# Kernel tuning notes

Hardware: AMD Instinct MI355X
Metric: run time of the kernel (lower is better)

The kernel has to match this reference:

```python
import jax, jax.numpy as jnp
import numpy as np

DIM = 1024
HEADS = 16
HEAD_DIM = DIM // HEADS
SCALE = HEAD_DIM ** -0.5
B, N = 2, 2048


def setup_inputs() -> dict:
    key = jax.random.key(0)
    ks = jax.random.split(key, 12)
    s = DIM ** -0.5
    return {
        "x_real": jax.random.normal(ks[0], (B, N, DIM), jnp.float32),
        "x_imag": jax.random.normal(ks[1], (B, N, DIM), jnp.float32),
        "Wqkv_r": jax.random.normal(ks[2], (3 * DIM, DIM), jnp.float32) * s,
        "bqkv_r": jax.random.normal(ks[3], (3 * DIM,), jnp.float32) * 0.01,
        "Wqkv_i": jax.random.normal(ks[4], (3 * DIM, DIM), jnp.float32) * s,
        "bqkv_i": jax.random.normal(ks[5], (3 * DIM,), jnp.float32) * 0.01,
        "Wout_r": jax.random.normal(ks[6], (DIM, DIM), jnp.float32) * s,
        "bout_r": jax.random.normal(ks[7], (DIM,), jnp.float32) * 0.01,
        "Wout_i": jax.random.normal(ks[8], (DIM, DIM), jnp.float32) * s,
        "bout_i": jax.random.normal(ks[9], (DIM,), jnp.float32) * 0.01,
    }


def _split_heads(qkv):
    # (B, N, 3*D) -> q, k, v each (B, H, N, hd)
    b, n, _ = qkv.shape
    qkv = qkv.reshape(b, n, 3, HEADS, HEAD_DIM).transpose(2, 0, 3, 1, 4)
    return qkv[0], qkv[1], qkv[2]


def reference(x_real, x_imag, Wqkv_r, bqkv_r, Wqkv_i, bqkv_i,
              Wout_r, bout_r, Wout_i, bout_i):
    b, n, d = x_real.shape
    q_r, k_r, v_r = _split_heads(x_real @ Wqkv_r.T + bqkv_r)
    q_i, k_i, v_i = _split_heads(x_imag @ Wqkv_i.T + bqkv_i)

    # complex score: (q_r + i q_i) (k_r - i k_i)^T pattern per source
    attn_real = (jnp.einsum('bhqd,bhkd->bhqk', q_r, k_r)
                 + jnp.einsum('bhqd,bhkd->bhqk', q_i, k_i)) * SCALE
    attn_imag = (jnp.einsum('bhqd,bhkd->bhqk', q_i, k_r)
                 - jnp.einsum('bhqd,bhkd->bhqk', q_r, k_i)) * SCALE
    attn_mag = jnp.sqrt(attn_real ** 2 + attn_imag ** 2)
    w = jax.nn.softmax(attn_mag, axis=-1)

    out_r = jnp.einsum('bhqk,bhkd->bhqd', w, v_r).transpose(0, 2, 1, 3).reshape(b, n, d)
    out_i = jnp.einsum('bhqk,bhkd->bhqd', w, v_i).transpose(0, 2, 1, 3).reshape(b, n, d)
    out_r = out_r @ Wout_r.T + bout_r
    out_i = out_i @ Wout_i.T + bout_i
    return out_r, out_i
```

## Files before the change

kernel.cpp:

```cpp
#include <hip/hip_runtime.h>


#define DIM_   1024
#define HEADS_ 16
#define HD_    64
#define BB_    2
#define NN_    2048
#define MTOT_  (BB_*NN_)
#define SCALE_ 0.125f

typedef __bf16 bf16;
typedef __bf16 bf16x8 __attribute__((ext_vector_type(8)));
typedef short  s16x8  __attribute__((ext_vector_type(8)));
typedef float  fx4    __attribute__((ext_vector_type(4)));

__device__ __forceinline__ bf16x8 neg8(bf16x8 v) {
    s16x8 s;
    __builtin_memcpy(&s, &v, sizeof(s));
    s ^= (short)0x8000;
    bf16x8 r;
    __builtin_memcpy(&r, &s, sizeof(r));
    return r;
}

__device__ __forceinline__ void gl_lds16(const void* g, void* l) {
    __builtin_amdgcn_global_load_lds(
        (const __attribute__((address_space(1))) unsigned int*)g,
        (__attribute__((address_space(3))) unsigned int*)l, 16, 0, 0);
}

__global__ __launch_bounds__(256) void qkv_gemm(
    const float* __restrict__ xr, const float* __restrict__ xi,
    const float* __restrict__ Wr, const float* __restrict__ Wi,
    const float* __restrict__ br, const float* __restrict__ bi,
    bf16* __restrict__ qbuf, bf16* __restrict__ kbuf, bf16* __restrict__ vbuf)
{
    const int z = blockIdx.z;
    const float* __restrict__ A    = z ? xi : xr;
    const float* __restrict__ W    = z ? Wi : Wr;
    const float* __restrict__ bias = z ? bi : br;
    const int n0 = blockIdx.x * 128;
    const int m0 = blockIdx.y * 128;

    __shared__ bf16 As[128*40];
    __shared__ bf16 Bs[128*40];

    const int tid  = threadIdx.x;
    const int w    = tid >> 6, lane = tid & 63;
    const int quad = lane >> 4, lc = lane & 15;
    const int wm   = (w >> 1) * 64, wn = (w & 1) * 64;

    const fx4 fzero = {0.f, 0.f, 0.f, 0.f};
    fx4 acc[4][4];
#pragma unroll
    for (int mi = 0; mi < 4; ++mi)
#pragma unroll
        for (int ni = 0; ni < 4; ++ni) acc[mi][ni] = fzero;

    for (int k0 = 0; k0 < DIM_; k0 += 32) {
#pragma unroll
        for (int it = 0; it < 2; ++it) {
            int flat = it*2048 + tid*8;
            int row = flat >> 5, col = flat & 31;
            const float* pa = A + (size_t)(m0+row)*DIM_ + k0 + col;
            const float* pb = W + (size_t)(n0+row)*DIM_ + k0 + col;
            fx4 a0 = *(const fx4*)pa, a1 = *(const fx4*)(pa+4);
            fx4 b0 = *(const fx4*)pb, b1 = *(const fx4*)(pb+4);
            bf16x8 av, bv;
#pragma unroll
            for (int j = 0; j < 4; ++j) {
                av[j] = (bf16)a0[j]; av[j+4] = (bf16)a1[j];
                bv[j] = (bf16)b0[j]; bv[j+4] = (bf16)b1[j];
            }
            *(bf16x8*)&As[row*40 + col] = av;
            *(bf16x8*)&Bs[row*40 + col] = bv;
        }
        __syncthreads();

        bf16x8 af[4], bfr[4];
#pragma unroll
        for (int mi = 0; mi < 4; ++mi) af[mi]  = *(bf16x8*)&As[(wm + mi*16 + lc)*40 + quad*8];
#pragma unroll
        for (int ni = 0; ni < 4; ++ni) bfr[ni] = *(bf16x8*)&Bs[(wn + ni*16 + lc)*40 + quad*8];
#pragma unroll
        for (int mi = 0; mi < 4; ++mi)
#pragma unroll
            for (int ni = 0; ni < 4; ++ni)
                acc[mi][ni] = __builtin_amdgcn_mfma_f32_16x16x32_bf16(af[mi], bfr[ni], acc[mi][ni], 0, 0, 0);
        __syncthreads();
    }

#pragma unroll
    for (int mi = 0; mi < 4; ++mi)
#pragma unroll
        for (int ni = 0; ni < 4; ++ni)
#pragma unroll
            for (int r = 0; r < 4; ++r) {
                int gm = m0 + wm + mi*16 + quad*4 + r;
                int gc = n0 + wn + ni*16 + lc;
                float val = acc[mi][ni][r] + bias[gc];
                bf16 bv = (bf16)val;
                int which = gc >> 10, h = (gc >> 6) & 15, hd = gc & 63;
                int b = gm >> 11, n = gm & 2047;
                size_t base = (size_t)((z*BB_ + b)*HEADS_ + h);
                if (which == 0)      qbuf[(base*NN_ + n)*HD_ + hd] = bv;
                else if (which == 1) kbuf[(base*NN_ + n)*HD_ + hd] = bv;
                else                 vbuf[(base*HD_ + hd)*NN_ + n] = bv;
            }
}

#define KT 32
#define NSTEP (NN_/KT)

__global__ __launch_bounds__(256, 2) void attn_fwd(
    const bf16* __restrict__ qbuf, const bf16* __restrict__ kbuf,
    const bf16* __restrict__ vbuf, bf16* __restrict__ obuf)
{
    const int bid = blockIdx.x;
    const int xcd = bid & 7;
    const int i   = bid >> 3;
    const int hb  = xcd*4 + (i >> 4);
    const int blk = i & 15;
    const int b = hb >> 4, h = hb & 15;

    const int tid  = threadIdx.x;
    const int w    = tid >> 6, lane = tid & 63;
    const int quad = lane >> 4, lc = lane & 15;
    const int q0   = blk*128 + w*32;

    __shared__ __align__(16) bf16 KV[2*8192];
    __shared__ __align__(16) bf16 Ps[4*2*32*40];
    bf16* psw = Ps + w*(2*32*40);

    const size_t hR = (size_t)(b)*HEADS_ + h;
    const size_t hI = (size_t)(BB_ + b)*HEADS_ + h;
    const bf16* qrg = qbuf + hR*NN_*HD_;
    const bf16* qig = qbuf + hI*NN_*HD_;
    const char* krg = (const char*)(kbuf + hR*NN_*HD_);
    const char* kig = (const char*)(kbuf + hI*NN_*HD_);
    const char* vrg = (const char*)(vbuf + hR*HD_*NN_);
    const char* vig = (const char*)(vbuf + hI*HD_*NN_);

    bf16x8 qr0[2], qr1[2], qi0[2], qi1[2], nqr0[2], nqr1[2];
#pragma unroll
    for (int band = 0; band < 2; ++band) {
        const bf16* pr = qrg + (size_t)(q0 + band*16 + lc)*HD_ + quad*8;
        const bf16* pi = qig + (size_t)(q0 + band*16 + lc)*HD_ + quad*8;
        qr0[band] = *(const bf16x8*)(pr);
        qr1[band] = *(const bf16x8*)(pr + 32);
        qi0[band] = *(const bf16x8*)(pi);
        qi1[band] = *(const bf16x8*)(pi + 32);
        nqr0[band] = neg8(qr0[band]);
        nqr1[band] = neg8(qr1[band]);
    }

    const char* stg_base;
    size_t lane_off, step_mul, j_mul;
    if (w < 2) {
        stg_base = w ? kig : krg;
        lane_off = (size_t)(lane >> 3)*128 + (size_t)((lane & 7) ^ (lane >> 3))*16;
        step_mul = (size_t)KT * 128;
        j_mul    = 1024;
    } else {
        stg_base = (w == 3) ? vig : vrg;
        lane_off = (size_t)(lane >> 2)*4096 + (size_t)((lane & 3) ^ ((lane >> 2) & 3))*16;
        step_mul = (size_t)KT * 2;
        j_mul    = 65536;
    }
    bf16* lds_arr = KV + w*2048;

    const fx4 fzero = {0.f, 0.f, 0.f, 0.f};
    fx4 O[2][2][4];
    float l_[2][4];
#pragma unroll
    for (int band = 0; band < 2; ++band) {
#pragma unroll
        for (int r = 0; r < 4; ++r) l_[band][r] = 0.f;
#pragma unroll
        for (int ri = 0; ri < 2; ++ri)
#pragma unroll
            for (int vb = 0; vb < 4; ++vb) O[band][ri][vb] = fzero;
    }
    bf16x8 pf[2];
    bf16x8 vf[2][4];

    {
        const char* g = stg_base + lane_off;
#pragma unroll
        for (int j = 0; j < 4; ++j)
            gl_lds16(g + j*j_mul, lds_arr + j*512);
    }
    __syncthreads();

    for (int s = 0; s < NSTEP; ++s) {
        const int buf = s & 1;
        bf16* kvb = KV + buf*8192;

        if (s < NSTEP-1) {
            const char* g = stg_base + (size_t)(s+1)*step_mul + lane_off;
            bf16* l = lds_arr + (buf ^ 1)*8192;
#pragma unroll
            for (int j = 0; j < 4; ++j)
                gl_lds16(g + j*j_mul, l + j*512);
        }

        if (s > 0) {
#pragma unroll
            for (int band = 0; band < 2; ++band)
#pragma unroll
                for (int ri = 0; ri < 2; ++ri)
#pragma unroll
                    for (int vb = 0; vb < 4; ++vb)
                        O[band][ri][vb] = __builtin_amdgcn_mfma_f32_16x16x32_bf16(
                            pf[band], vf[ri][vb], O[band][ri][vb], 0, 0, 0);
        }

        bf16x8 kr_[2][2], ki_[2][2];
#pragma unroll
        for (int kb = 0; kb < 2; ++kb)
#pragma unroll
            for (int half = 0; half < 2; ++half) {
                int r = kb*16 + lc;
                int c = (half*4 + quad) ^ (r & 7);
                kr_[kb][half] = *(bf16x8*)&kvb[0*2048 + r*64 + c*8];
                ki_[kb][half] = *(bf16x8*)&kvb[1*2048 + r*64 + c*8];
            }

#pragma unroll
        for (int band = 0; band < 2; ++band)
#pragma unroll
            for (int kb = 0; kb < 2; ++kb) {
                fx4 sr = fzero, si = fzero;
                sr = __builtin_amdgcn_mfma_f32_16x16x32_bf16(qr0[band],  kr_[kb][0], sr, 0,0,0);
                sr = __builtin_amdgcn_mfma_f32_16x16x32_bf16(qr1[band],  kr_[kb][1], sr, 0,0,0);
                sr = __builtin_amdgcn_mfma_f32_16x16x32_bf16(qi0[band],  ki_[kb][0], sr, 0,0,0);
                sr = __builtin_amdgcn_mfma_f32_16x16x32_bf16(qi1[band],  ki_[kb][1], sr, 0,0,0);
                si = __builtin_amdgcn_mfma_f32_16x16x32_bf16(qi0[band],  kr_[kb][0], si, 0,0,0);
                si = __builtin_amdgcn_mfma_f32_16x16x32_bf16(qi1[band],  kr_[kb][1], si, 0,0,0);
                si = __builtin_amdgcn_mfma_f32_16x16x32_bf16(nqr0[band], ki_[kb][0], si, 0,0,0);
                si = __builtin_amdgcn_mfma_f32_16x16x32_bf16(nqr1[band], ki_[kb][1], si, 0,0,0);
#pragma unroll
                for (int r = 0; r < 4; ++r) {
                    float s2 = sr[r]*sr[r] + si[r]*si[r];
                    float mg = __builtin_amdgcn_sqrtf(s2);
                    float pv = __expf(mg * SCALE_);
                    l_[band][r] += pv;
                    psw[buf*1280 + (band*16 + quad*4 + r)*40 + kb*16 + lc] = (bf16)pv;
                }
            }

#pragma unroll
        for (int band = 0; band < 2; ++band)
            pf[band] = *(bf16x8*)&psw[buf*1280 + (band*16 + lc)*40 + quad*8];
#pragma unroll
        for (int ri = 0; ri < 2; ++ri)
#pragma unroll
            for (int vb = 0; vb < 4; ++vb) {
                int r = vb*16 + lc;
                int c = quad ^ (r & 3);
                vf[ri][vb] = *(bf16x8*)&kvb[(2+ri)*2048 + r*32 + c*8];
            }

        __syncthreads();
    }

#pragma unroll
    for (int band = 0; band < 2; ++band)
#pragma unroll
        for (int ri = 0; ri < 2; ++ri)
#pragma unroll
            for (int vb = 0; vb < 4; ++vb)
                O[band][ri][vb] = __builtin_amdgcn_mfma_f32_16x16x32_bf16(
                    pf[band], vf[ri][vb], O[band][ri][vb], 0, 0, 0);

#pragma unroll
    for (int off = 1; off < 16; off <<= 1)
#pragma unroll
        for (int band = 0; band < 2; ++band)
#pragma unroll
            for (int r = 0; r < 4; ++r)
                l_[band][r] += __shfl_xor(l_[band][r], off);
    float inv[2][4];
#pragma unroll
    for (int band = 0; band < 2; ++band)
#pragma unroll
        for (int r = 0; r < 4; ++r) inv[band][r] = 1.f / l_[band][r];

    bf16* obr = obuf + ((size_t)(b)*NN_)*DIM_;
    bf16* obi = obuf + ((size_t)(BB_ + b)*NN_)*DIM_;
#pragma unroll
    for (int band = 0; band < 2; ++band)
#pragma unroll
        for (int vb = 0; vb < 4; ++vb)
#pragma unroll
            for (int r = 0; r < 4; ++r) {
                int gn = q0 + band*16 + quad*4 + r;
                int gc = h*HD_ + vb*16 + lc;
                obr[(size_t)gn*DIM_ + gc] = (bf16)(O[band][0][vb][r] * inv[band][r]);
                obi[(size_t)gn*DIM_ + gc] = (bf16)(O[band][1][vb][r] * inv[band][r]);
            }
}

__global__ __launch_bounds__(256) void out_gemm(
    const bf16* __restrict__ obuf,
    const float* __restrict__ Wr, const float* __restrict__ Wi,
    const float* __restrict__ br, const float* __restrict__ bi,
    float* __restrict__ out)
{
    const int z = blockIdx.z;
    const bf16*  __restrict__ A    = obuf + (size_t)z * MTOT_ * DIM_;
    const float* __restrict__ W    = z ? Wi : Wr;
    const float* __restrict__ bias = z ? bi : br;
    float* __restrict__ dst        = out + (size_t)z * MTOT_ * DIM_;
    const int n0 = blockIdx.x * 128;
    const int m0 = blockIdx.y * 128;

    __shared__ bf16 As[128*40];
    __shared__ bf16 Bs[128*40];

    const int tid  = threadIdx.x;
    const int w    = tid >> 6, lane = tid & 63;
    const int quad = lane >> 4, lc = lane & 15;
    const int wm   = (w >> 1) * 64, wn = (w & 1) * 64;

    const fx4 fzero = {0.f, 0.f, 0.f, 0.f};
    fx4 acc[4][4];
#pragma unroll
    for (int mi = 0; mi < 4; ++mi)
#pragma unroll
        for (int ni = 0; ni < 4; ++ni) acc[mi][ni] = fzero;

    for (int k0 = 0; k0 < DIM_; k0 += 32) {
#pragma unroll
        for (int it = 0; it < 2; ++it) {
            int flat = it*2048 + tid*8;
            int row = flat >> 5, col = flat & 31;
            *(bf16x8*)&As[row*40 + col] = *(const bf16x8*)(A + (size_t)(m0+row)*DIM_ + k0 + col);
            const float* pb = W + (size_t)(n0+row)*DIM_ + k0 + col;
            fx4 b0 = *(const fx4*)pb, b1 = *(const fx4*)(pb+4);
            bf16x8 bv;
#pragma unroll
            for (int j = 0; j < 4; ++j) { bv[j] = (bf16)b0[j]; bv[j+4] = (bf16)b1[j]; }
            *(bf16x8*)&Bs[row*40 + col] = bv;
        }
        __syncthreads();

        bf16x8 af[4], bfr[4];
#pragma unroll
        for (int mi = 0; mi < 4; ++mi) af[mi]  = *(bf16x8*)&As[(wm + mi*16 + lc)*40 + quad*8];
#pragma unroll
        for (int ni = 0; ni < 4; ++ni) bfr[ni] = *(bf16x8*)&Bs[(wn + ni*16 + lc)*40 + quad*8];
#pragma unroll
        for (int mi = 0; mi < 4; ++mi)
#pragma unroll
            for (int ni = 0; ni < 4; ++ni)
                acc[mi][ni] = __builtin_amdgcn_mfma_f32_16x16x32_bf16(af[mi], bfr[ni], acc[mi][ni], 0, 0, 0);
        __syncthreads();
    }

#pragma unroll
    for (int mi = 0; mi < 4; ++mi)
#pragma unroll
        for (int ni = 0; ni < 4; ++ni)
#pragma unroll
            for (int r = 0; r < 4; ++r) {
                int gm = m0 + wm + mi*16 + quad*4 + r;
                int gc = n0 + wn + ni*16 + lc;
                dst[(size_t)gm*DIM_ + gc] = acc[mi][ni][r] + bias[gc];
            }
}

extern "C" void kernel_launch(void* const* d_in, const int* in_sizes, int n_in,
                              void* d_out, int out_size, void* d_ws, size_t ws_size,
                              hipStream_t stream) {
    const float* xr  = (const float*)d_in[0];
    const float* xi  = (const float*)d_in[1];
    const float* Wqr = (const float*)d_in[2];
    const float* bqr = (const float*)d_in[3];
    const float* Wqi = (const float*)d_in[4];
    const float* bqi = (const float*)d_in[5];
    const float* Wor = (const float*)d_in[6];
    const float* bor = (const float*)d_in[7];
    const float* Woi = (const float*)d_in[8];
    const float* boi = (const float*)d_in[9];
    float* out = (float*)d_out;

    bf16* ws = (bf16*)d_ws;
    const size_t per = (size_t)2 * BB_ * HEADS_ * NN_ * HD_;
    bf16* qbuf = ws;
    bf16* kbuf = ws + per;
    bf16* vbuf = ws + 2*per;
    bf16* obuf = ws + 3*per;

    qkv_gemm<<<dim3(24, 32, 2), 256, 0, stream>>>(xr, xi, Wqr, Wqi, bqr, bqi, qbuf, kbuf, vbuf);
    attn_fwd<<<dim3(512), 256, 0, stream>>>(qbuf, kbuf, vbuf, obuf);
    out_gemm<<<dim3(8, 32, 2), 256, 0, stream>>>(obuf, Wor, Woi, bor, boi, out);
}
```

Baseline: 369.5 us.

## Pre-convert inputs and weights to bf16 and use LDS-DMA swizzled GEMMs

```diff
diff --git a/kernel.cpp b/kernel.cpp
--- a/kernel.cpp
+++ b/kernel.cpp
@@ -29,66 +29,87 @@
         (__attribute__((address_space(3))) unsigned int*)l, 16, 0, 0);
 }
 
-__global__ __launch_bounds__(256) void qkv_gemm(
+__global__ __launch_bounds__(256) void cvt_prepass(
     const float* __restrict__ xr, const float* __restrict__ xi,
-    const float* __restrict__ Wr, const float* __restrict__ Wi,
+    const float* __restrict__ wqr, const float* __restrict__ wqi,
+    const float* __restrict__ wor, const float* __restrict__ woi,
+    bf16* __restrict__ xbf, bf16* __restrict__ wqkv, bf16* __restrict__ wout)
+{
+    const int bid = blockIdx.x;
+    const float* src; bf16* dst; int rel;
+    if      (bid < 2048) { src = xr;  dst = xbf;           rel = bid; }
+    else if (bid < 4096) { src = xi;  dst = xbf + 4194304; rel = bid - 2048; }
+    else if (bid < 5632) { src = wqr; dst = wqkv;          rel = bid - 4096; }
+    else if (bid < 7168) { src = wqi; dst = wqkv + 3145728; rel = bid - 5632; }
+    else if (bid < 7680) { src = wor; dst = wout;          rel = bid - 7168; }
+    else                 { src = woi; dst = wout + 1048576; rel = bid - 7680; }
+    size_t base = (size_t)rel * 2048 + (size_t)threadIdx.x * 8;
+    fx4 a = *(const fx4*)(src + base);
+    fx4 b = *(const fx4*)(src + base + 4);
+    bf16x8 o;
+#pragma unroll
+    for (int j = 0; j < 4; ++j) { o[j] = (bf16)a[j]; o[j+4] = (bf16)b[j]; }
+    *(bf16x8*)(dst + base) = o;
+}
+
+#define GEMM_CORE(Aptr, Bptr)                                                  \
+    __shared__ __align__(16) bf16 As[128*64];                                  \
+    __shared__ __align__(16) bf16 Bs[128*64];                                  \
+    const int tid  = threadIdx.x;                                              \
+    const int w    = tid >> 6, lane = tid & 63;                                \
+    const int quad = lane >> 4, lc = lane & 15;                                \
+    const int wm   = (w >> 1) * 64, wn = (w & 1) * 64;                         \
+    const int rj   = lane >> 3;                                                \
+    const int sc   = (lane & 7) ^ rj;                                          \
+    const fx4 fzero = {0.f, 0.f, 0.f, 0.f};                                    \
+    fx4 acc[4][4];                                                             \
+    _Pragma("unroll")                                                          \
+    for (int mi = 0; mi < 4; ++mi)                                             \
+        _Pragma("unroll")                                                      \
+        for (int ni = 0; ni < 4; ++ni) acc[mi][ni] = fzero;                    \
+    for (int k0 = 0; k0 < DIM_; k0 += 64) {                                    \
+        _Pragma("unroll")                                                      \
+        for (int j = 0; j < 4; ++j) {                                          \
+            int grp = j*4 + w;                                                 \
+            int gr  = grp*8 + rj;                                              \
+            gl_lds16(Aptr + (size_t)(m0+gr)*DIM_ + k0 + sc*8, As + grp*512);   \
+            gl_lds16(Bptr + (size_t)(n0+gr)*DIM_ + k0 + sc*8, Bs + grp*512);   \
+        }                                                                      \
+        __syncthreads();                                                       \
+        bf16x8 af[2][4], bfr[2][4];                                            \
+        _Pragma("unroll")                                                      \
+        for (int ks = 0; ks < 2; ++ks) {                                       \
+            _Pragma("unroll")                                                  \
+            for (int mi = 0; mi < 4; ++mi)                                     \
+                af[ks][mi] = *(bf16x8*)&As[(wm+mi*16+lc)*64 + (((ks*4+quad)^(lc&7))*8)]; \
+            _Pragma("unroll")                                                  \
+            for (int ni = 0; ni < 4; ++ni)                                     \
+                bfr[ks][ni] = *(bf16x8*)&Bs[(wn+ni*16+lc)*64 + (((ks*4+quad)^(lc&7))*8)]; \
+        }                                                                      \
+        _Pragma("unroll")                                                      \
+        for (int ks = 0; ks < 2; ++ks)                                         \
+            _Pragma("unroll")                                                  \
+            for (int mi = 0; mi < 4; ++mi)                                     \
+                _Pragma("unroll")                                              \
+                for (int ni = 0; ni < 4; ++ni)                                 \
+                    acc[mi][ni] = __builtin_amdgcn_mfma_f32_16x16x32_bf16(     \
+                        af[ks][mi], bfr[ks][ni], acc[mi][ni], 0, 0, 0);        \
+        __syncthreads();                                                       \
+    }
+
+__global__ __launch_bounds__(256) void qkv_gemm_dma(
+    const bf16* __restrict__ xbf, const bf16* __restrict__ wqkv,
     const float* __restrict__ br, const float* __restrict__ bi,
     bf16* __restrict__ qbuf, bf16* __restrict__ kbuf, bf16* __restrict__ vbuf)
 {
     const int z = blockIdx.z;
-    const float* __restrict__ A    = z ? xi : xr;
-    const float* __restrict__ W    = z ? Wi : Wr;
+    const bf16* __restrict__ Ap = xbf  + (size_t)z * 4194304;
+    const bf16* __restrict__ Bp = wqkv + (size_t)z * 3145728;
     const float* __restrict__ bias = z ? bi : br;
     const int n0 = blockIdx.x * 128;
     const int m0 = blockIdx.y * 128;
 
-    __shared__ bf16 As[128*40];
-    __shared__ bf16 Bs[128*40];
-
-    const int tid  = threadIdx.x;
-    const int w    = tid >> 6, lane = tid & 63;
-    const int quad = lane >> 4, lc = lane & 15;
-    const int wm   = (w >> 1) * 64, wn = (w & 1) * 64;
-
-    const fx4 fzero = {0.f, 0.f, 0.f, 0.f};
-    fx4 acc[4][4];
-#pragma unroll
-    for (int mi = 0; mi < 4; ++mi)
-#pragma unroll
-        for (int ni = 0; ni < 4; ++ni) acc[mi][ni] = fzero;
-
-    for (int k0 = 0; k0 < DIM_; k0 += 32) {
-#pragma unroll
-        for (int it = 0; it < 2; ++it) {
-            int flat = it*2048 + tid*8;
-            int row = flat >> 5, col = flat & 31;
-            const float* pa = A + (size_t)(m0+row)*DIM_ + k0 + col;
-            const float* pb = W + (size_t)(n0+row)*DIM_ + k0 + col;
-            fx4 a0 = *(const fx4*)pa, a1 = *(const fx4*)(pa+4);
-            fx4 b0 = *(const fx4*)pb, b1 = *(const fx4*)(pb+4);
-            bf16x8 av, bv;
-#pragma unroll
-            for (int j = 0; j < 4; ++j) {
-                av[j] = (bf16)a0[j]; av[j+4] = (bf16)a1[j];
-                bv[j] = (bf16)b0[j]; bv[j+4] = (bf16)b1[j];
-            }
-            *(bf16x8*)&As[row*40 + col] = av;
-            *(bf16x8*)&Bs[row*40 + col] = bv;
-        }
-        __syncthreads();
-
-        bf16x8 af[4], bfr[4];
-#pragma unroll
-        for (int mi = 0; mi < 4; ++mi) af[mi]  = *(bf16x8*)&As[(wm + mi*16 + lc)*40 + quad*8];
-#pragma unroll
-        for (int ni = 0; ni < 4; ++ni) bfr[ni] = *(bf16x8*)&Bs[(wn + ni*16 + lc)*40 + quad*8];
-#pragma unroll
-        for (int mi = 0; mi < 4; ++mi)
-#pragma unroll
-            for (int ni = 0; ni < 4; ++ni)
-                acc[mi][ni] = __builtin_amdgcn_mfma_f32_16x16x32_bf16(af[mi], bfr[ni], acc[mi][ni], 0, 0, 0);
-        __syncthreads();
-    }
+    GEMM_CORE(Ap, Bp)
 
 #pragma unroll
     for (int mi = 0; mi < 4; ++mi)
@@ -106,6 +127,33 @@
                 if (which == 0)      qbuf[(base*NN_ + n)*HD_ + hd] = bv;
                 else if (which == 1) kbuf[(base*NN_ + n)*HD_ + hd] = bv;
                 else                 vbuf[(base*HD_ + hd)*NN_ + n] = bv;
+            }
+}
+
+__global__ __launch_bounds__(256) void out_gemm_dma(
+    const bf16* __restrict__ obuf, const bf16* __restrict__ wout,
+    const float* __restrict__ br, const float* __restrict__ bi,
+    float* __restrict__ out)
+{
+    const int z = blockIdx.z;
+    const bf16* __restrict__ Ap = obuf + (size_t)z * 4194304;
+    const bf16* __restrict__ Bp = wout + (size_t)z * 1048576;
+    const float* __restrict__ bias = z ? bi : br;
+    float* __restrict__ dst = out + (size_t)z * 4194304;
+    const int n0 = blockIdx.x * 128;
+    const int m0 = blockIdx.y * 128;
+
+    GEMM_CORE(Ap, Bp)
+
+#pragma unroll
+    for (int mi = 0; mi < 4; ++mi)
+#pragma unroll
+        for (int ni = 0; ni < 4; ++ni)
+#pragma unroll
+            for (int r = 0; r < 4; ++r) {
+                int gm = m0 + wm + mi*16 + quad*4 + r;
+                int gc = n0 + wn + ni*16 + lc;
+                dst[(size_t)gm*DIM_ + gc] = acc[mi][ni][r] + bias[gc];
             }
 }
 
@@ -301,7 +349,87 @@
             }
 }
 
-__global__ __launch_bounds__(256) void out_gemm(
+__global__ __launch_bounds__(256) void qkv_gemm_legacy(
+    const float* __restrict__ xr, const float* __restrict__ xi,
+    const float* __restrict__ Wr, const float* __restrict__ Wi,
+    const float* __restrict__ br, const float* __restrict__ bi,
+    bf16* __restrict__ qbuf, bf16* __restrict__ kbuf, bf16* __restrict__ vbuf)
+{
+    const int z = blockIdx.z;
+    const float* __restrict__ A    = z ? xi : xr;
+    const float* __restrict__ W    = z ? Wi : Wr;
+    const float* __restrict__ bias = z ? bi : br;
+    const int n0 = blockIdx.x * 128;
+    const int m0 = blockIdx.y * 128;
+
+    __shared__ bf16 As[128*40];
+    __shared__ bf16 Bs[128*40];
+
+    const int tid  = threadIdx.x;
+    const int w    = tid >> 6, lane = tid & 63;
+    const int quad = lane >> 4, lc = lane & 15;
+    const int wm   = (w >> 1) * 64, wn = (w & 1) * 64;
+
+    const fx4 fzero = {0.f, 0.f, 0.f, 0.f};
+    fx4 acc[4][4];
+#pragma unroll
+    for (int mi = 0; mi < 4; ++mi)
+#pragma unroll
+        for (int ni = 0; ni < 4; ++ni) acc[mi][ni] = fzero;
+
+    for (int k0 = 0; k0 < DIM_; k0 += 32) {
+#pragma unroll
+        for (int it = 0; it < 2; ++it) {
+            int flat = it*2048 + tid*8;
+            int row = flat >> 5, col = flat & 31;
+            const float* pa = A + (size_t)(m0+row)*DIM_ + k0 + col;
+            const float* pb = W + (size_t)(n0+row)*DIM_ + k0 + col;
+            fx4 a0 = *(const fx4*)pa, a1 = *(const fx4*)(pa+4);
+            fx4 b0 = *(const fx4*)pb, b1 = *(const fx4*)(pb+4);
+            bf16x8 av, bv;
+#pragma unroll
+            for (int j = 0; j < 4; ++j) {
+                av[j] = (bf16)a0[j]; av[j+4] = (bf16)a1[j];
+                bv[j] = (bf16)b0[j]; bv[j+4] = (bf16)b1[j];
+            }
+            *(bf16x8*)&As[row*40 + col] = av;
+            *(bf16x8*)&Bs[row*40 + col] = bv;
+        }
+        __syncthreads();
+
+        bf16x8 af[4], bfr[4];
+#pragma unroll
+        for (int mi = 0; mi < 4; ++mi) af[mi]  = *(bf16x8*)&As[(wm + mi*16 + lc)*40 + quad*8];
+#pragma unroll
+        for (int ni = 0; ni < 4; ++ni) bfr[ni] = *(bf16x8*)&Bs[(wn + ni*16 + lc)*40 + quad*8];
+#pragma unroll
+        for (int mi = 0; mi < 4; ++mi)
+#pragma unroll
+            for (int ni = 0; ni < 4; ++ni)
+                acc[mi][ni] = __builtin_amdgcn_mfma_f32_16x16x32_bf16(af[mi], bfr[ni], acc[mi][ni], 0, 0, 0);
+        __syncthreads();
+    }
+
+#pragma unroll
+    for (int mi = 0; mi < 4; ++mi)
+#pragma unroll
+        for (int ni = 0; ni < 4; ++ni)
+#pragma unroll
+            for (int r = 0; r < 4; ++r) {
+                int gm = m0 + wm + mi*16 + quad*4 + r;
+                int gc = n0 + wn + ni*16 + lc;
+                float val = acc[mi][ni][r] + bias[gc];
+                bf16 bv = (bf16)val;
+                int which = gc >> 10, h = (gc >> 6) & 15, hd = gc & 63;
+                int b = gm >> 11, n = gm & 2047;
+                size_t base = (size_t)((z*BB_ + b)*HEADS_ + h);
+                if (which == 0)      qbuf[(base*NN_ + n)*HD_ + hd] = bv;
+                else if (which == 1) kbuf[(base*NN_ + n)*HD_ + hd] = bv;
+                else                 vbuf[(base*HD_ + hd)*NN_ + n] = bv;
+            }
+}
+
+__global__ __launch_bounds__(256) void out_gemm_legacy(
     const bf16* __restrict__ obuf,
     const float* __restrict__ Wr, const float* __restrict__ Wi,
     const float* __restrict__ br, const float* __restrict__ bi,
@@ -386,13 +514,33 @@
     float* out = (float*)d_out;
 
     bf16* ws = (bf16*)d_ws;
-    const size_t per = (size_t)2 * BB_ * HEADS_ * NN_ * HD_;
-    bf16* qbuf = ws;
-    bf16* kbuf = ws + per;
-    bf16* vbuf = ws + 2*per;
-    bf16* obuf = ws + 3*per;
-
-    qkv_gemm<<<dim3(24, 32, 2), 256, 0, stream>>>(xr, xi, Wqr, Wqi, bqr, bqi, qbuf, kbuf, vbuf);
-    attn_fwd<<<dim3(512), 256, 0, stream>>>(qbuf, kbuf, vbuf, obuf);
-    out_gemm<<<dim3(8, 32, 2), 256, 0, stream>>>(obuf, Wor, Woi, bor, boi, out);
-}
+    const size_t NEED = 83886080ull;
+
+    if (ws_size >= NEED) {
+        bf16* xbf  = ws;
+        bf16* wqkv = ws + 8388608;
+        bf16* wout = ws + 14680064;
+        bf16* qb   = ws + 16777216;
+        bf16* kb   = ws + 25165824;
+        bf16* vb   = ws + 33554432;
+        bf16* obuf = xbf;
+
+        cvt_prepass<<<dim3(8192), 256, 0, stream>>>(xr, xi, Wqr, Wqi, Wor, Woi,
+                                                    xbf, wqkv, wout);
+        qkv_gemm_dma<<<dim3(24, 32, 2), 256, 0, stream>>>(xbf, wqkv, bqr, bqi,
+                                                          qb, kb, vb);
+        attn_fwd<<<dim3(512), 256, 0, stream>>>(qb, kb, vb, obuf);
+        out_gemm_dma<<<dim3(8, 32, 2), 256, 0, stream>>>(obuf, wout, bor, boi, out);
+    } else {
+        const size_t per = (size_t)2 * BB_ * HEADS_ * NN_ * HD_;
+        bf16* qb   = ws;
+        bf16* kb   = ws + per;
+        bf16* vb   = ws + 2*per;
+        bf16* obuf = ws + 3*per;
+        qkv_gemm_legacy<<<dim3(24, 32, 2), 256, 0, stream>>>(xr, xi, Wqr, Wqi,
+                                                             bqr, bqi, qb, kb, vb);
+        attn_fwd<<<dim3(512), 256, 0, stream>>>(qb, kb, vb, obuf);
+        out_gemm_legacy<<<dim3(8, 32, 2), 256, 0, stream>>>(obuf, Wor, Woi,
+                                                            bor, boi, out);
+    }
+}
```

After: 351.3 us. -4.9%, faster.
